# Kernel optimization log

Measured on AMD Instinct MI355X. Metric: run time of the kernel, lower is better.

The kernel has to match this reference:

```python
import jax, jax.numpy as jnp
import numpy as np

N_AGENTS = 32
STATE_DIM = 6 * N_AGENTS      # 192
CONTROL_DIM = 3 * N_AGENTS    # 96
HIDDEN = 100
NEWTON_ITERS = 40

# Index maps from the cvxpy objective:
#   p[u_x_r]^T u[u_idx] + p[u_y_r]^T u[2*u_idx] + p[u_z_r]^T u[3*u_idx]
_u_idx = np.arange(N_AGENTS)
P_IDX = np.concatenate([3 * np.arange(1, N_AGENTS + 1),
                        4 * np.arange(1, N_AGENTS + 1),
                        5 * np.arange(1, N_AGENTS + 1)])
U_IDX = np.concatenate([_u_idx, 2 * _u_idx, 3 * _u_idx])


def _p_net(t, z, W1, b1, W2, b2, W3, b3):
    # DefaultPNet: MLP on concat([t, z]) with tanh hiddens (hidden_dim=100)
    x = jnp.concatenate([t, z], axis=-1)          # [B, 1+STATE_DIM]
    h = jnp.tanh(x @ W1 + b1)
    h = jnp.tanh(h @ W2 + b2)
    return h @ W3 + b3                            # [B, STATE_DIM]


def _solve_qp(q):
    # min_u q^T u + 0.5||u||^2 + 0.25||u||^4  (unconstrained, strictly convex)
    # Stationarity: q + (1+||u||^2) u = 0 => u = -q/(1+s), s = ||u||^2
    # => s (1+s)^2 = ||q||^2 ; solve scalar cubic per row via Newton.
    r = jnp.sum(q * q, axis=-1)                   # [B]
    s0 = jnp.cbrt(r)                              # good init: s ~ r^(1/3) for large r

    def step(s, _):
        one = 1.0 + s
        f = s * one * one - r
        fp = one * one + 2.0 * s * one
        return jnp.maximum(s - f / fp, 0.0), None

    s, _ = jax.lax.scan(step, s0, None, length=NEWTON_ITERS)
    return -q / (1.0 + s)[:, None]                # [B, CONTROL_DIM]


def setup_inputs() -> dict:
    key = jax.random.key(0)
    ks = jax.random.split(key, 8)
    B = 131072
    in_dim = 1 + STATE_DIM
    sc1 = 1.0 / np.sqrt(in_dim)
    sc2 = 1.0 / np.sqrt(HIDDEN)
    return {
        "z": jax.random.normal(ks[0], (B, STATE_DIM), jnp.float32),
        "t": jax.random.uniform(ks[1], (B, 1), jnp.float32),
        "W1": jax.random.normal(ks[2], (in_dim, HIDDEN), jnp.float32) * sc1,
        "b1": jnp.zeros((HIDDEN,), jnp.float32),
        "W2": jax.random.normal(ks[3], (HIDDEN, HIDDEN), jnp.float32) * sc2,
        "b2": jnp.zeros((HIDDEN,), jnp.float32),
        "W3": jax.random.normal(ks[4], (HIDDEN, STATE_DIM), jnp.float32) * sc2,
        "b3": jnp.zeros((STATE_DIM,), jnp.float32),
    }


def reference(z, t, W1, b1, W2, b2, W3, b3):
    p = _p_net(t, z, W1, b1, W2, b2, W3, b3)      # [B, STATE_DIM]
    # Accumulate linear coefficients onto u (indices overlap, so scatter-add)
    q = jnp.zeros((p.shape[0], CONTROL_DIM), p.dtype).at[:, U_IDX].add(p[:, P_IDX])
    return _solve_qp(q)                            # ustar [B, CONTROL_DIM]
```

## Files before the change

### kernel.cpp

```cpp
#include <hip/hip_runtime.h>
#include <hip/hip_bf16.h>


typedef __attribute__((ext_vector_type(8))) short short8;
typedef __attribute__((ext_vector_type(4))) float f32x4;

__device__ __forceinline__ unsigned short f2bf(float f) {
  unsigned u = __float_as_uint(f);
  u += 0x7fffu + ((u >> 16) & 1u);
  return (unsigned short)(u >> 16);
}
__device__ __forceinline__ float tanh_fast(float x) {
  float e = __builtin_amdgcn_exp2f(x * 2.88539008177792681f);
  return fmaf(-2.f, __builtin_amdgcn_rcpf(e + 1.f), 1.f);
}
__device__ __forceinline__ short8 pack_bf8(f32x4 a, f32x4 b) {
  union { short8 s; __hip_bfloat162 h[4]; } u;
  u.h[0] = __float22bfloat162_rn(make_float2(a[0], a[1]));
  u.h[1] = __float22bfloat162_rn(make_float2(a[2], a[3]));
  u.h[2] = __float22bfloat162_rn(make_float2(b[0], b[1]));
  u.h[3] = __float22bfloat162_rn(make_float2(b[2], b[3]));
  return u.s;
}
__device__ __forceinline__ unsigned pk2u(float lo, float hi) {
  union { __hip_bfloat162 h; unsigned u; } x;
  x.h = __float22bfloat162_rn(make_float2(lo, hi));
  return x.u;
}

__global__ void cvx_prep(const float* __restrict__ W1, const float* __restrict__ b1,
                         const float* __restrict__ W2, const float* __restrict__ b2,
                         const float* __restrict__ W3, const float* __restrict__ b3,
                         short* __restrict__ pw) {
  int idx = blockIdx.x * 256 + threadIdx.x;

  if (idx < 21504) {
    int kt = idx / 3584, rem = idx % 3584;
    int nt = rem / 512, e = rem % 512;
    int lane = e >> 3, j = e & 7;
    int k = kt * 32 + (lane >> 4) * 8 + j;
    int n = nt * 16 + (lane & 15);
    float wv = (n < 100) ? W1[(k + 1) * 100 + n] : 0.f;
    pw[(kt * 7 + nt) * 512 + e] = (short)f2bf(wv);
    return;
  }
  idx -= 21504;
  if (idx < 14336) {
    int kt = idx / 3584, rem = idx % 3584;
    int nt = rem / 512, e = rem % 512;
    int lane = e >> 3, j = e & 7;
    int k = kt * 32 + (lane >> 4) * 8 + j;
    int n = nt * 16 + (lane & 15);
    float wv = (k < 100 && n < 100) ? W2[k * 100 + n] : 0.f;
    pw[21504 + (kt * 7 + nt) * 512 + e] = (short)f2bf(wv);
    return;
  }
  idx -= 14336;
  if (idx < 12288) {
    int kt = idx / 3072, rem = idx % 3072;
    int nt = rem / 512, e = rem % 512;
    int lane = e >> 3, j = e & 7;
    int k = kt * 32 + (lane >> 4) * 8 + j;
    int u = nt * 16 + (lane & 15);
    float wv = 0.f;
    if (k < 100) {
      const float* wr = W3 + k * 192;
      if (u <= 31) wv += wr[3 * u + 3];
      if ((u & 1) == 0 && u <= 62) wv += wr[2 * u + 4];
      if (u % 3 == 0 && u <= 93) wv += wr[(5 * u) / 3 + 5];
    }
    pw[35840 + (kt * 6 + nt) * 512 + e] = (short)f2bf(wv);
    return;
  }
  idx -= 12288;
  float* cb = (float*)(pw + 48128);
  if (idx < 112) { cb[idx] = (idx < 100) ? W1[idx] : 0.f; return; }
  idx -= 112;
  if (idx < 112) { cb[112 + idx] = (idx < 100) ? b1[idx] : 0.f; return; }
  idx -= 112;
  if (idx < 112) { cb[224 + idx] = (idx < 100) ? b2[idx] : 0.f; return; }
  idx -= 112;
  if (idx < 96) {
    int u = idx;
    float v = 0.f;
    if (u <= 31) v += b3[3 * u + 3];
    if ((u & 1) == 0 && u <= 62) v += b3[2 * u + 4];
    if (u % 3 == 0 && u <= 93) v += b3[(5 * u) / 3 + 5];
    cb[336 + u] = v;
  }
}

__global__ __launch_bounds__(512, 1) void cvx_main(
    const float* __restrict__ zin, const float* __restrict__ tin,
    const short* __restrict__ pw, float* __restrict__ out) {
  __shared__ __align__(16) short wbuf[48128];
  __shared__ __align__(16) float cbl[448];

  const int tid = threadIdx.x;
  const int wid = tid >> 6;
  const int lane = tid & 63;
  const int l15 = lane & 15;
  const int qd = lane >> 4;
  const int lo_src = ((lane & 16) << 1) + l15;
  const int hi_src = lo_src + 16;
  const bool selA = lane < 32;

  for (int f = wid; f < 94; f += 8) {
    const short* g = pw + f * 512 + lane * 8;
    __builtin_amdgcn_global_load_lds(
        (const __attribute__((address_space(1))) void*)g,
        (__attribute__((address_space(3))) void*)&wbuf[f * 512], 16, 0, 0);
  }
  if (tid < 448) cbl[tid] = ((const float*)(pw + 48128))[tid];

  const int row0 = blockIdx.x * 512 + wid * 64;

  short8 XB[4][6];
  float tc[4];
#pragma unroll
  for (int bt = 0; bt < 4; bt++) {
    const float* zr = zin + (size_t)(row0 + bt * 16 + l15) * 192 + qd * 8;
#pragma unroll
    for (int kt = 0; kt < 6; kt++) {
      f32x4 a = *(const f32x4*)(zr + kt * 32);
      f32x4 b = *(const f32x4*)(zr + kt * 32 + 4);
      XB[bt][kt] = pack_bf8(a, b);
    }
    tc[bt] = tin[row0 + bt * 16 + l15];
  }

  __syncthreads();

  auto buildHB = [&](const unsigned (&pkb)[7][2], int kt) -> short8 {
    union { short8 s; unsigned u[4]; } hb;
    if (kt < 3) {
      unsigned a0 = (unsigned)__shfl((int)pkb[2 * kt][0], lo_src);
      unsigned b0 = (unsigned)__shfl((int)pkb[2 * kt + 1][0], lo_src);
      unsigned a1 = (unsigned)__shfl((int)pkb[2 * kt][1], lo_src);
      unsigned b1_ = (unsigned)__shfl((int)pkb[2 * kt + 1][1], lo_src);
      unsigned a2 = (unsigned)__shfl((int)pkb[2 * kt][0], hi_src);
      unsigned b2_ = (unsigned)__shfl((int)pkb[2 * kt + 1][0], hi_src);
      unsigned a3 = (unsigned)__shfl((int)pkb[2 * kt][1], hi_src);
      unsigned b3_ = (unsigned)__shfl((int)pkb[2 * kt + 1][1], hi_src);
      hb.u[0] = selA ? a0 : b0;
      hb.u[1] = selA ? a1 : b1_;
      hb.u[2] = selA ? a2 : b2_;
      hb.u[3] = selA ? a3 : b3_;
    } else {
      hb.u[0] = (unsigned)__shfl((int)pkb[6][0], lo_src);
      hb.u[1] = (unsigned)__shfl((int)pkb[6][1], lo_src);
      hb.u[2] = (unsigned)__shfl((int)pkb[6][0], hi_src);
      hb.u[3] = (unsigned)__shfl((int)pkb[6][1], hi_src);
    }
    return hb.s;
  };

  f32x4 acc[4][7];
#pragma unroll
  for (int bt = 0; bt < 4; bt++)
#pragma unroll
    for (int nt = 0; nt < 7; nt++) {
      f32x4 zzz = {0.f, 0.f, 0.f, 0.f};
      acc[bt][nt] = zzz;
    }
#pragma unroll
  for (int kt = 0; kt < 6; kt++)
#pragma unroll
    for (int nt = 0; nt < 7; nt++) {
      short8 wf = *(const short8*)&wbuf[(kt * 7 + nt) * 512 + lane * 8];
      acc[0][nt] = __builtin_amdgcn_mfma_f32_16x16x32_bf16(wf, XB[0][kt], acc[0][nt], 0, 0, 0);
      acc[1][nt] = __builtin_amdgcn_mfma_f32_16x16x32_bf16(wf, XB[1][kt], acc[1][nt], 0, 0, 0);
      acc[2][nt] = __builtin_amdgcn_mfma_f32_16x16x32_bf16(wf, XB[2][kt], acc[2][nt], 0, 0, 0);
      acc[3][nt] = __builtin_amdgcn_mfma_f32_16x16x32_bf16(wf, XB[3][kt], acc[3][nt], 0, 0, 0);
    }

  unsigned pk[4][7][2];
#pragma unroll
  for (int bt = 0; bt < 4; bt++)
#pragma unroll
    for (int nt = 0; nt < 7; nt++) {
      f32x4 w0v = *(const f32x4*)&cbl[nt * 16 + qd * 4];
      f32x4 b1v = *(const f32x4*)&cbl[112 + nt * 16 + qd * 4];
#pragma unroll
      for (int r = 0; r < 4; r++)
        acc[bt][nt][r] = tanh_fast(fmaf(tc[bt], w0v[r], acc[bt][nt][r] + b1v[r]));
      pk[bt][nt][0] = pk2u(acc[bt][nt][0], acc[bt][nt][1]);
      pk[bt][nt][1] = pk2u(acc[bt][nt][2], acc[bt][nt][3]);
    }

#pragma unroll
  for (int bt = 0; bt < 4; bt++)
#pragma unroll
    for (int nt = 0; nt < 7; nt++) {
      f32x4 zzz = {0.f, 0.f, 0.f, 0.f};
      acc[bt][nt] = zzz;
    }
#pragma unroll
  for (int kt = 0; kt < 4; kt++) {
    short8 hb0 = buildHB(pk[0], kt);
    short8 hb1 = buildHB(pk[1], kt);
    short8 hb2 = buildHB(pk[2], kt);
    short8 hb3 = buildHB(pk[3], kt);
#pragma unroll
    for (int nt = 0; nt < 7; nt++) {
      short8 wf = *(const short8*)&wbuf[(42 + kt * 7 + nt) * 512 + lane * 8];
      acc[0][nt] = __builtin_amdgcn_mfma_f32_16x16x32_bf16(wf, hb0, acc[0][nt], 0, 0, 0);
      acc[1][nt] = __builtin_amdgcn_mfma_f32_16x16x32_bf16(wf, hb1, acc[1][nt], 0, 0, 0);
      acc[2][nt] = __builtin_amdgcn_mfma_f32_16x16x32_bf16(wf, hb2, acc[2][nt], 0, 0, 0);
      acc[3][nt] = __builtin_amdgcn_mfma_f32_16x16x32_bf16(wf, hb3, acc[3][nt], 0, 0, 0);
    }
  }
#pragma unroll
  for (int bt = 0; bt < 4; bt++)
#pragma unroll
    for (int nt = 0; nt < 7; nt++) {
      f32x4 b2v = *(const f32x4*)&cbl[224 + nt * 16 + qd * 4];
#pragma unroll
      for (int r = 0; r < 4; r++)
        acc[bt][nt][r] = tanh_fast(acc[bt][nt][r] + b2v[r]);
      pk[bt][nt][0] = pk2u(acc[bt][nt][0], acc[bt][nt][1]);
      pk[bt][nt][1] = pk2u(acc[bt][nt][2], acc[bt][nt][3]);
    }

  f32x4 qa[4][6];
#pragma unroll
  for (int bt = 0; bt < 4; bt++)
#pragma unroll
    for (int nt = 0; nt < 6; nt++) {
      f32x4 zzz = {0.f, 0.f, 0.f, 0.f};
      qa[bt][nt] = zzz;
    }
#pragma unroll
  for (int kt = 0; kt < 4; kt++) {
    short8 hb0 = buildHB(pk[0], kt);
    short8 hb1 = buildHB(pk[1], kt);
    short8 hb2 = buildHB(pk[2], kt);
    short8 hb3 = buildHB(pk[3], kt);
#pragma unroll
    for (int nt = 0; nt < 6; nt++) {
      short8 wf = *(const short8*)&wbuf[(70 + kt * 6 + nt) * 512 + lane * 8];
      qa[0][nt] = __builtin_amdgcn_mfma_f32_16x16x32_bf16(wf, hb0, qa[0][nt], 0, 0, 0);
      qa[1][nt] = __builtin_amdgcn_mfma_f32_16x16x32_bf16(wf, hb1, qa[1][nt], 0, 0, 0);
      qa[2][nt] = __builtin_amdgcn_mfma_f32_16x16x32_bf16(wf, hb2, qa[2][nt], 0, 0, 0);
      qa[3][nt] = __builtin_amdgcn_mfma_f32_16x16x32_bf16(wf, hb3, qa[3][nt], 0, 0, 0);
    }
  }

#pragma unroll
  for (int bt = 0; bt < 4; bt++) {
#pragma unroll
    for (int nt = 0; nt < 6; nt++) {
      f32x4 bqv = *(const f32x4*)&cbl[336 + nt * 16 + qd * 4];
      qa[bt][nt] += bqv;
    }
    float loc = 0.f;
#pragma unroll
    for (int nt = 0; nt < 6; nt++) {
      f32x4 q = qa[bt][nt];
      loc += q[0] * q[0] + q[1] * q[1] + q[2] * q[2] + q[3] * q[3];
    }
    loc += __shfl_xor(loc, 16);
    loc += __shfl_xor(loc, 32);
    float r2 = loc;
    float s = __builtin_amdgcn_exp2f(__builtin_amdgcn_logf(r2) * 0.333333333333f);
#pragma unroll
    for (int itn = 0; itn < 8; itn++) {
      float one = 1.f + s;
      float fv = fmaf(s * one, one, -r2);
      float fp = one * fmaf(2.f, s, one);
      s = fmaxf(s - fv * __builtin_amdgcn_rcpf(fp), 0.f);
    }
    float inv = -__builtin_amdgcn_rcpf(1.f + s);
    float* orow = out + (size_t)(row0 + bt * 16 + l15) * 96;
#pragma unroll
    for (int nt = 0; nt < 6; nt++) {
      f32x4 v = qa[bt][nt] * inv;
      *(f32x4*)(orow + nt * 16 + qd * 4) = v;
    }
  }
}

extern "C" void kernel_launch(void* const* d_in, const int* in_sizes, int n_in,
                              void* d_out, int out_size, void* d_ws, size_t ws_size,
                              hipStream_t stream) {
  const float* z  = (const float*)d_in[0];
  const float* t  = (const float*)d_in[1];
  const float* W1 = (const float*)d_in[2];
  const float* b1 = (const float*)d_in[3];
  const float* W2 = (const float*)d_in[4];
  const float* b2 = (const float*)d_in[5];
  const float* W3 = (const float*)d_in[6];
  const float* b3 = (const float*)d_in[7];
  float* out = (float*)d_out;
  int B = in_sizes[0] / 192;

  short* pw = (short*)d_ws;
  cvx_prep<<<190, 256, 0, stream>>>(W1, b1, W2, b2, W3, b3, pw);
  cvx_main<<<B / 512, 512, 0, stream>>>(z, t, pw, out);
}
```

Measured before the change: 193.4 us.

## Read MFMA weight fragments directly from global memory and shrink blocks for occupancy

Drops the per-block LDS staging of the packed bf16 weights and constants, so each wave reads weight fragments and biases straight from global memory (relying on L1/L2 caching). Blocks shrink to 256 threads with 32 rows per wave and launch bounds of (256,4). The aim is to remove the large LDS copy, the barrier and the single-block-per-CU limit so more waves overlap. In exchange every MFMA weight operand becomes a global load with higher latency, and weight traffic per row doubles because each wave now covers half as many rows.

```diff
diff --git a/kernel.cpp b/kernel.cpp
--- a/kernel.cpp
+++ b/kernel.cpp
@@ -90,12 +90,9 @@
   }
 }
 
-__global__ __launch_bounds__(512, 1) void cvx_main(
+__global__ __launch_bounds__(256, 4) void cvx_main(
     const float* __restrict__ zin, const float* __restrict__ tin,
     const short* __restrict__ pw, float* __restrict__ out) {
-  __shared__ __align__(16) short wbuf[48128];
-  __shared__ __align__(16) float cbl[448];
-
   const int tid = threadIdx.x;
   const int wid = tid >> 6;
   const int lane = tid & 63;
@@ -105,20 +102,14 @@
   const int hi_src = lo_src + 16;
   const bool selA = lane < 32;
 
-  for (int f = wid; f < 94; f += 8) {
-    const short* g = pw + f * 512 + lane * 8;
-    __builtin_amdgcn_global_load_lds(
-        (const __attribute__((address_space(1))) void*)g,
-        (__attribute__((address_space(3))) void*)&wbuf[f * 512], 16, 0, 0);
-  }
-  if (tid < 448) cbl[tid] = ((const float*)(pw + 48128))[tid];
-
-  const int row0 = blockIdx.x * 512 + wid * 64;
-
-  short8 XB[4][6];
-  float tc[4];
-#pragma unroll
-  for (int bt = 0; bt < 4; bt++) {
+  const int row0 = blockIdx.x * 128 + wid * 32;
+  const short* wfrag = pw + lane * 8;
+  const float* cb = (const float*)(pw + 48128);
+
+  short8 XB[2][6];
+  float tc[2];
+#pragma unroll
+  for (int bt = 0; bt < 2; bt++) {
     const float* zr = zin + (size_t)(row0 + bt * 16 + l15) * 192 + qd * 8;
 #pragma unroll
     for (int kt = 0; kt < 6; kt++) {
@@ -128,8 +119,6 @@
     }
     tc[bt] = tin[row0 + bt * 16 + l15];
   }
-
-  __syncthreads();
 
   auto buildHB = [&](const unsigned (&pkb)[7][2], int kt) -> short8 {
     union { short8 s; unsigned u[4]; } hb;
@@ -155,32 +144,28 @@
     return hb.s;
   };
 
-  f32x4 acc[4][7];
-#pragma unroll
-  for (int bt = 0; bt < 4; bt++)
-#pragma unroll
-    for (int nt = 0; nt < 7; nt++) {
-      f32x4 zzz = {0.f, 0.f, 0.f, 0.f};
-      acc[bt][nt] = zzz;
-    }
+  f32x4 acc[2][7];
+#pragma unroll
+  for (int nt = 0; nt < 7; nt++) {
+    f32x4 zzz = {0.f, 0.f, 0.f, 0.f};
+    acc[0][nt] = zzz; acc[1][nt] = zzz;
+  }
 #pragma unroll
   for (int kt = 0; kt < 6; kt++)
 #pragma unroll
     for (int nt = 0; nt < 7; nt++) {
-      short8 wf = *(const short8*)&wbuf[(kt * 7 + nt) * 512 + lane * 8];
+      short8 wf = *(const short8*)(wfrag + (kt * 7 + nt) * 512);
       acc[0][nt] = __builtin_amdgcn_mfma_f32_16x16x32_bf16(wf, XB[0][kt], acc[0][nt], 0, 0, 0);
       acc[1][nt] = __builtin_amdgcn_mfma_f32_16x16x32_bf16(wf, XB[1][kt], acc[1][nt], 0, 0, 0);
-      acc[2][nt] = __builtin_amdgcn_mfma_f32_16x16x32_bf16(wf, XB[2][kt], acc[2][nt], 0, 0, 0);
-      acc[3][nt] = __builtin_amdgcn_mfma_f32_16x16x32_bf16(wf, XB[3][kt], acc[3][nt], 0, 0, 0);
-    }
-
-  unsigned pk[4][7][2];
-#pragma unroll
-  for (int bt = 0; bt < 4; bt++)
-#pragma unroll
-    for (int nt = 0; nt < 7; nt++) {
-      f32x4 w0v = *(const f32x4*)&cbl[nt * 16 + qd * 4];
-      f32x4 b1v = *(const f32x4*)&cbl[112 + nt * 16 + qd * 4];
+    }
+
+  unsigned pk[2][7][2];
+#pragma unroll
+  for (int bt = 0; bt < 2; bt++)
+#pragma unroll
+    for (int nt = 0; nt < 7; nt++) {
+      f32x4 w0v = *(const f32x4*)&cb[nt * 16 + qd * 4];
+      f32x4 b1v = *(const f32x4*)&cb[112 + nt * 16 + qd * 4];
 #pragma unroll
       for (int r = 0; r < 4; r++)
         acc[bt][nt][r] = tanh_fast(fmaf(tc[bt], w0v[r], acc[bt][nt][r] + b1v[r]));
@@ -189,32 +174,26 @@
     }
 
 #pragma unroll
-  for (int bt = 0; bt < 4; bt++)
-#pragma unroll
-    for (int nt = 0; nt < 7; nt++) {
-      f32x4 zzz = {0.f, 0.f, 0.f, 0.f};
-      acc[bt][nt] = zzz;
-    }
+  for (int nt = 0; nt < 7; nt++) {
+    f32x4 zzz = {0.f, 0.f, 0.f, 0.f};
+    acc[0][nt] = zzz; acc[1][nt] = zzz;
+  }
 #pragma unroll
   for (int kt = 0; kt < 4; kt++) {
     short8 hb0 = buildHB(pk[0], kt);
     short8 hb1 = buildHB(pk[1], kt);
-    short8 hb2 = buildHB(pk[2], kt);
-    short8 hb3 = buildHB(pk[3], kt);
-#pragma unroll
-    for (int nt = 0; nt < 7; nt++) {
-      short8 wf = *(const short8*)&wbuf[(42 + kt * 7 + nt) * 512 + lane * 8];
+#pragma unroll
+    for (int nt = 0; nt < 7; nt++) {
+      short8 wf = *(const short8*)(wfrag + (42 + kt * 7 + nt) * 512);
       acc[0][nt] = __builtin_amdgcn_mfma_f32_16x16x32_bf16(wf, hb0, acc[0][nt], 0, 0, 0);
       acc[1][nt] = __builtin_amdgcn_mfma_f32_16x16x32_bf16(wf, hb1, acc[1][nt], 0, 0, 0);
-      acc[2][nt] = __builtin_amdgcn_mfma_f32_16x16x32_bf16(wf, hb2, acc[2][nt], 0, 0, 0);
-      acc[3][nt] = __builtin_amdgcn_mfma_f32_16x16x32_bf16(wf, hb3, acc[3][nt], 0, 0, 0);
-    }
-  }
-#pragma unroll
-  for (int bt = 0; bt < 4; bt++)
-#pragma unroll
-    for (int nt = 0; nt < 7; nt++) {
-      f32x4 b2v = *(const f32x4*)&cbl[224 + nt * 16 + qd * 4];
+    }
+  }
+#pragma unroll
+  for (int bt = 0; bt < 2; bt++)
+#pragma unroll
+    for (int nt = 0; nt < 7; nt++) {
+      f32x4 b2v = *(const f32x4*)&cb[224 + nt * 16 + qd * 4];
 #pragma unroll
       for (int r = 0; r < 4; r++)
         acc[bt][nt][r] = tanh_fast(acc[bt][nt][r] + b2v[r]);
@@ -222,35 +201,29 @@
       pk[bt][nt][1] = pk2u(acc[bt][nt][2], acc[bt][nt][3]);
     }
 
-  f32x4 qa[4][6];
-#pragma unroll
-  for (int bt = 0; bt < 4; bt++)
-#pragma unroll
-    for (int nt = 0; nt < 6; nt++) {
-      f32x4 zzz = {0.f, 0.f, 0.f, 0.f};
-      qa[bt][nt] = zzz;
-    }
+  f32x4 qa[2][6];
+#pragma unroll
+  for (int nt = 0; nt < 6; nt++) {
+    f32x4 zzz = {0.f, 0.f, 0.f, 0.f};
+    qa[0][nt] = zzz; qa[1][nt] = zzz;
+  }
 #pragma unroll
   for (int kt = 0; kt < 4; kt++) {
     short8 hb0 = buildHB(pk[0], kt);
     short8 hb1 = buildHB(pk[1], kt);
-    short8 hb2 = buildHB(pk[2], kt);
-    short8 hb3 = buildHB(pk[3], kt);
-#pragma unroll
-    for (int nt = 0; nt < 6; nt++) {
-      short8 wf = *(const short8*)&wbuf[(70 + kt * 6 + nt) * 512 + lane * 8];
+#pragma unroll
+    for (int nt = 0; nt < 6; nt++) {
+      short8 wf = *(const short8*)(wfrag + (70 + kt * 6 + nt) * 512);
       qa[0][nt] = __builtin_amdgcn_mfma_f32_16x16x32_bf16(wf, hb0, qa[0][nt], 0, 0, 0);
       qa[1][nt] = __builtin_amdgcn_mfma_f32_16x16x32_bf16(wf, hb1, qa[1][nt], 0, 0, 0);
-      qa[2][nt] = __builtin_amdgcn_mfma_f32_16x16x32_bf16(wf, hb2, qa[2][nt], 0, 0, 0);
-      qa[3][nt] = __builtin_amdgcn_mfma_f32_16x16x32_bf16(wf, hb3, qa[3][nt], 0, 0, 0);
-    }
-  }
-
-#pragma unroll
-  for (int bt = 0; bt < 4; bt++) {
-#pragma unroll
-    for (int nt = 0; nt < 6; nt++) {
-      f32x4 bqv = *(const f32x4*)&cbl[336 + nt * 16 + qd * 4];
+    }
+  }
+
+#pragma unroll
+  for (int bt = 0; bt < 2; bt++) {
+#pragma unroll
+    for (int nt = 0; nt < 6; nt++) {
+      f32x4 bqv = *(const f32x4*)&cb[336 + nt * 16 + qd * 4];
       qa[bt][nt] += bqv;
     }
     float loc = 0.f;
@@ -296,5 +269,5 @@
 
   short* pw = (short*)d_ws;
   cvx_prep<<<190, 256, 0, stream>>>(W1, b1, W2, b2, W3, b3, pw);
-  cvx_main<<<B / 512, 512, 0, stream>>>(z, t, pw, out);
-}
+  cvx_main<<<B / 128, 256, 0, stream>>>(z, t, pw, out);
+}
```

Result: slower. 199.4 us (+3.1%).

## Process row tiles in a loop with software-prefetched inputs and two blocks per CU

Applied to the files above, without the earlier changes.

Each wave now handles one 16-row tile per iteration of a four-step loop instead of four tiles at once, and loads the next tile's z and t rows into registers while computing the current one. This lowers register pressure enough to raise launch bounds to two blocks per CU, so global loads can overlap with MFMA work. The trade-off is that each weight fragment read from LDS now feeds only one MFMA instead of four, which raises LDS traffic. Two blocks per CU also need about 96KB of LDS per block pair, which may or may not fit.

```diff
diff --git a/kernel.cpp b/kernel.cpp
--- a/kernel.cpp
+++ b/kernel.cpp
@@ -90,7 +90,7 @@
   }
 }
 
-__global__ __launch_bounds__(512, 1) void cvx_main(
+__global__ __launch_bounds__(512, 2) void cvx_main(
     const float* __restrict__ zin, const float* __restrict__ tin,
     const short* __restrict__ pw, float* __restrict__ out) {
   __shared__ __align__(16) short wbuf[48128];
@@ -113,20 +113,18 @@
   }
   if (tid < 448) cbl[tid] = ((const float*)(pw + 48128))[tid];
 
-  const int row0 = blockIdx.x * 512 + wid * 64;
-
-  short8 XB[4][6];
-  float tc[4];
-#pragma unroll
-  for (int bt = 0; bt < 4; bt++) {
-    const float* zr = zin + (size_t)(row0 + bt * 16 + l15) * 192 + qd * 8;
+  const int rowb = blockIdx.x * 512;
+
+  f32x4 sga[6], sgb[6];
+  float tld;
+  {
+    const float* zr = zin + (size_t)(rowb + wid * 16 + l15) * 192 + qd * 8;
 #pragma unroll
     for (int kt = 0; kt < 6; kt++) {
-      f32x4 a = *(const f32x4*)(zr + kt * 32);
-      f32x4 b = *(const f32x4*)(zr + kt * 32 + 4);
-      XB[bt][kt] = pack_bf8(a, b);
-    }
-    tc[bt] = tin[row0 + bt * 16 + l15];
+      sga[kt] = *(const f32x4*)(zr + kt * 32);
+      sgb[kt] = *(const f32x4*)(zr + kt * 32 + 4);
+    }
+    tld = tin[rowb + wid * 16 + l15];
   }
 
   __syncthreads();
@@ -155,108 +153,101 @@
     return hb.s;
   };
 
-  f32x4 acc[4][7];
-#pragma unroll
-  for (int bt = 0; bt < 4; bt++)
+#pragma unroll 1
+  for (int it = 0; it < 4; ++it) {
+    const int row0 = rowb + it * 128 + wid * 16;
+
+    short8 XB[6];
+#pragma unroll
+    for (int kt = 0; kt < 6; kt++) XB[kt] = pack_bf8(sga[kt], sgb[kt]);
+    float tc = tld;
+
+    if (it < 3) {
+      const float* zr = zin + (size_t)(row0 + 128 + l15) * 192 + qd * 8;
+#pragma unroll
+      for (int kt = 0; kt < 6; kt++) {
+        sga[kt] = *(const f32x4*)(zr + kt * 32);
+        sgb[kt] = *(const f32x4*)(zr + kt * 32 + 4);
+      }
+      tld = tin[row0 + 128 + l15];
+      __builtin_amdgcn_sched_barrier(0);
+    }
+
+    f32x4 acc[7];
 #pragma unroll
     for (int nt = 0; nt < 7; nt++) {
       f32x4 zzz = {0.f, 0.f, 0.f, 0.f};
-      acc[bt][nt] = zzz;
-    }
-#pragma unroll
-  for (int kt = 0; kt < 6; kt++)
-#pragma unroll
-    for (int nt = 0; nt < 7; nt++) {
-      short8 wf = *(const short8*)&wbuf[(kt * 7 + nt) * 512 + lane * 8];
-      acc[0][nt] = __builtin_amdgcn_mfma_f32_16x16x32_bf16(wf, XB[0][kt], acc[0][nt], 0, 0, 0);
-      acc[1][nt] = __builtin_amdgcn_mfma_f32_16x16x32_bf16(wf, XB[1][kt], acc[1][nt], 0, 0, 0);
-      acc[2][nt] = __builtin_amdgcn_mfma_f32_16x16x32_bf16(wf, XB[2][kt], acc[2][nt], 0, 0, 0);
-      acc[3][nt] = __builtin_amdgcn_mfma_f32_16x16x32_bf16(wf, XB[3][kt], acc[3][nt], 0, 0, 0);
-    }
-
-  unsigned pk[4][7][2];
-#pragma unroll
-  for (int bt = 0; bt < 4; bt++)
+      acc[nt] = zzz;
+    }
+#pragma unroll
+    for (int kt = 0; kt < 6; kt++)
+#pragma unroll
+      for (int nt = 0; nt < 7; nt++) {
+        short8 wf = *(const short8*)&wbuf[(kt * 7 + nt) * 512 + lane * 8];
+        acc[nt] = __builtin_amdgcn_mfma_f32_16x16x32_bf16(wf, XB[kt], acc[nt], 0, 0, 0);
+      }
+
+    unsigned pk[7][2];
 #pragma unroll
     for (int nt = 0; nt < 7; nt++) {
       f32x4 w0v = *(const f32x4*)&cbl[nt * 16 + qd * 4];
       f32x4 b1v = *(const f32x4*)&cbl[112 + nt * 16 + qd * 4];
 #pragma unroll
       for (int r = 0; r < 4; r++)
-        acc[bt][nt][r] = tanh_fast(fmaf(tc[bt], w0v[r], acc[bt][nt][r] + b1v[r]));
-      pk[bt][nt][0] = pk2u(acc[bt][nt][0], acc[bt][nt][1]);
-      pk[bt][nt][1] = pk2u(acc[bt][nt][2], acc[bt][nt][3]);
-    }
-
-#pragma unroll
-  for (int bt = 0; bt < 4; bt++)
+        acc[nt][r] = tanh_fast(fmaf(tc, w0v[r], acc[nt][r] + b1v[r]));
+      pk[nt][0] = pk2u(acc[nt][0], acc[nt][1]);
+      pk[nt][1] = pk2u(acc[nt][2], acc[nt][3]);
+    }
+
 #pragma unroll
     for (int nt = 0; nt < 7; nt++) {
       f32x4 zzz = {0.f, 0.f, 0.f, 0.f};
-      acc[bt][nt] = zzz;
-    }
-#pragma unroll
-  for (int kt = 0; kt < 4; kt++) {
-    short8 hb0 = buildHB(pk[0], kt);
-    short8 hb1 = buildHB(pk[1], kt);
-    short8 hb2 = buildHB(pk[2], kt);
-    short8 hb3 = buildHB(pk[3], kt);
-#pragma unroll
-    for (int nt = 0; nt < 7; nt++) {
-      short8 wf = *(const short8*)&wbuf[(42 + kt * 7 + nt) * 512 + lane * 8];
-      acc[0][nt] = __builtin_amdgcn_mfma_f32_16x16x32_bf16(wf, hb0, acc[0][nt], 0, 0, 0);
-      acc[1][nt] = __builtin_amdgcn_mfma_f32_16x16x32_bf16(wf, hb1, acc[1][nt], 0, 0, 0);
-      acc[2][nt] = __builtin_amdgcn_mfma_f32_16x16x32_bf16(wf, hb2, acc[2][nt], 0, 0, 0);
-      acc[3][nt] = __builtin_amdgcn_mfma_f32_16x16x32_bf16(wf, hb3, acc[3][nt], 0, 0, 0);
-    }
-  }
-#pragma unroll
-  for (int bt = 0; bt < 4; bt++)
+      acc[nt] = zzz;
+    }
+#pragma unroll
+    for (int kt = 0; kt < 4; kt++) {
+      short8 hb = buildHB(pk, kt);
+#pragma unroll
+      for (int nt = 0; nt < 7; nt++) {
+        short8 wf = *(const short8*)&wbuf[(42 + kt * 7 + nt) * 512 + lane * 8];
+        acc[nt] = __builtin_amdgcn_mfma_f32_16x16x32_bf16(wf, hb, acc[nt], 0, 0, 0);
+      }
+    }
 #pragma unroll
     for (int nt = 0; nt < 7; nt++) {
       f32x4 b2v = *(const f32x4*)&cbl[224 + nt * 16 + qd * 4];
 #pragma unroll
       for (int r = 0; r < 4; r++)
-        acc[bt][nt][r] = tanh_fast(acc[bt][nt][r] + b2v[r]);
-      pk[bt][nt][0] = pk2u(acc[bt][nt][0], acc[bt][nt][1]);
-      pk[bt][nt][1] = pk2u(acc[bt][nt][2], acc[bt][nt][3]);
-    }
-
-  f32x4 qa[4][6];
-#pragma unroll
-  for (int bt = 0; bt < 4; bt++)
+        acc[nt][r] = tanh_fast(acc[nt][r] + b2v[r]);
+      pk[nt][0] = pk2u(acc[nt][0], acc[nt][1]);
+      pk[nt][1] = pk2u(acc[nt][2], acc[nt][3]);
+    }
+
+    f32x4 qa[6];
 #pragma unroll
     for (int nt = 0; nt < 6; nt++) {
       f32x4 zzz = {0.f, 0.f, 0.f, 0.f};
-      qa[bt][nt] = zzz;
-    }
-#pragma unroll
-  for (int kt = 0; kt < 4; kt++) {
-    short8 hb0 = buildHB(pk[0], kt);
-    short8 hb1 = buildHB(pk[1], kt);
-    short8 hb2 = buildHB(pk[2], kt);
-    short8 hb3 = buildHB(pk[3], kt);
-#pragma unroll
-    for (int nt = 0; nt < 6; nt++) {
-      short8 wf = *(const short8*)&wbuf[(70 + kt * 6 + nt) * 512 + lane * 8];
-      qa[0][nt] = __builtin_amdgcn_mfma_f32_16x16x32_bf16(wf, hb0, qa[0][nt], 0, 0, 0);
-      qa[1][nt] = __builtin_amdgcn_mfma_f32_16x16x32_bf16(wf, hb1, qa[1][nt], 0, 0, 0);
-      qa[2][nt] = __builtin_amdgcn_mfma_f32_16x16x32_bf16(wf, hb2, qa[2][nt], 0, 0, 0);
-      qa[3][nt] = __builtin_amdgcn_mfma_f32_16x16x32_bf16(wf, hb3, qa[3][nt], 0, 0, 0);
-    }
-  }
-
-#pragma unroll
-  for (int bt = 0; bt < 4; bt++) {
+      qa[nt] = zzz;
+    }
+#pragma unroll
+    for (int kt = 0; kt < 4; kt++) {
+      short8 hb = buildHB(pk, kt);
+#pragma unroll
+      for (int nt = 0; nt < 6; nt++) {
+        short8 wf = *(const short8*)&wbuf[(70 + kt * 6 + nt) * 512 + lane * 8];
+        qa[nt] = __builtin_amdgcn_mfma_f32_16x16x32_bf16(wf, hb, qa[nt], 0, 0, 0);
+      }
+    }
+
 #pragma unroll
     for (int nt = 0; nt < 6; nt++) {
       f32x4 bqv = *(const f32x4*)&cbl[336 + nt * 16 + qd * 4];
-      qa[bt][nt] += bqv;
+      qa[nt] += bqv;
     }
     float loc = 0.f;
 #pragma unroll
     for (int nt = 0; nt < 6; nt++) {
-      f32x4 q = qa[bt][nt];
+      f32x4 q = qa[nt];
       loc += q[0] * q[0] + q[1] * q[1] + q[2] * q[2] + q[3] * q[3];
     }
     loc += __shfl_xor(loc, 16);
@@ -271,10 +262,10 @@
       s = fmaxf(s - fv * __builtin_amdgcn_rcpf(fp), 0.f);
     }
     float inv = -__builtin_amdgcn_rcpf(1.f + s);
-    float* orow = out + (size_t)(row0 + bt * 16 + l15) * 96;
-#pragma unroll
-    for (int nt = 0; nt < 6; nt++) {
-      f32x4 v = qa[bt][nt] * inv;
+    float* orow = out + (size_t)(row0 + l15) * 96;
+#pragma unroll
+    for (int nt = 0; nt < 6; nt++) {
+      f32x4 v = qa[nt] * inv;
       *(f32x4*)(orow + nt * 16 + qd * 4) = v;
     }
   }
```

New measurement: 185.5 us. 4.1% less time.
